# Kernel optimization log

Measured on AMD Instinct MI355X. Metric: run time of the kernel, lower is better.

## Reference

```python
import jax, jax.numpy as jnp
import numpy as np
from jax import lax

# module hyperparams (from init_kwargs)
K = 7
STRIDE = 1
PAD = 3
DIL = 1


def setup_inputs() -> dict:
    key = jax.random.key(0)
    ks = jax.random.split(key, 5)
    B, Cin, Cout, L = 4, 256, 256, 8192
    x = jax.random.normal(ks[0], (B, Cin, L), jnp.float32)
    # main conv weight (Cout, Cin, K), kaiming-ish scale
    weight = jax.random.normal(ks[1], (Cout, Cin, K), jnp.float32) * (1.0 / np.sqrt(Cin * K))
    bias = jax.random.normal(ks[2], (Cout,), jnp.float32) * 0.01
    # offset conv: Conv1d(Cin -> K, kernel K); small values so sampling is perturbed but in-range
    offset_w = jax.random.normal(ks[3], (K, Cin, K), jnp.float32) * 0.01
    offset_b = jax.random.normal(ks[4], (K,), jnp.float32) * 0.01
    return {"x": x, "weight": weight, "bias": bias, "offset_w": offset_w, "offset_b": offset_b}


def reference(x, weight, bias, offset_w, offset_b):
    B, Cin, L = x.shape
    out_len = (L + 2 * PAD - DIL * (K - 1) - 1) // STRIDE + 1

    # offset conv: (B, Cin, L) -> (B, K, out_len)
    offsets = lax.conv_general_dilated(
        x, offset_w, window_strides=(STRIDE,), padding=[(PAD, PAD)],
        rhs_dilation=(DIL,), dimension_numbers=("NCH", "OIH", "NCH"))
    offsets = offsets + offset_b[None, :, None]
    offsets = jnp.transpose(offsets, (0, 2, 1))  # (B, out_len, K)

    # standard sampling locations (1, out_len, K), shifted by padding as in original
    p = jnp.arange(out_len, dtype=jnp.float32)[None, :, None] * STRIDE
    p_k = (jnp.arange(K, dtype=jnp.float32) - (K - 1) / 2.0) * DIL
    loc = p + p_k[None, None, :] + PAD + offsets  # (B, out_len, K)

    # linear interpolation (clamped endpoints, matching torch clamp order)
    x0 = jnp.floor(loc).astype(jnp.int32)
    x1 = x0 + 1
    x0c = jnp.clip(x0, 0, L - 1)
    x1c = jnp.clip(x1, 0, L - 1)
    wa = x1c.astype(jnp.float32) - loc  # weights use clamped indices, as original
    wb = loc - x0c.astype(jnp.float32)

    # gather: per batch, (Cin, L)[:, (out_len, K)] -> (Cin, out_len, K)
    gather = jax.vmap(lambda xb, ib: xb[:, ib])
    fa = gather(x, x0c)  # (B, Cin, out_len, K)
    fb = gather(x, x1c)
    interp = wa[:, None] * fa + wb[:, None] * fb  # (B, Cin, out_len, K)

    # einsum 'blki,oik->blo' with interp laid out as (B, i=Cin, l, k)
    out = jnp.einsum("bilk,oik->bol", interp, weight) + bias[None, :, None]
    return out
```

## Files before the change

kernel.cpp:

```cpp
#include <hip/hip_runtime.h>
#include <hip/hip_bf16.h>


#define B_    4
#define CIN   256
#define COUT  256
#define LEN   8192
#define KK    7
#define NTOT  (B_ * LEN)
#define QTOT  (CIN * KK)
#define LPITCH 232

typedef short s16x8 __attribute__((ext_vector_type(8)));
typedef int   s32x4 __attribute__((ext_vector_type(4)));
typedef float f32x4 __attribute__((ext_vector_type(4)));

static __device__ __forceinline__ unsigned f2bf(float f) {
  union { float f; unsigned u; } u; u.f = f;
  unsigned r = u.u + 0x7FFF + ((u.u >> 16) & 1);
  return r >> 16;
}

static __device__ __forceinline__ int cvt_pk_bf16(float a, float b) {
  int r;
  asm("v_cvt_pk_bf16_f32 %0, %1, %2" : "=v"(r) : "v"(a), "v"(b));
  return r;
}

__global__ __launch_bounds__(256) void loc_partial(
    const float* __restrict__ X, const float* __restrict__ OW,
    float* __restrict__ Partial) {
  __shared__ float red[4][256][KK];

  const int t    = threadIdx.x;
  const int lane = t & 63;
  const int wu   = __builtin_amdgcn_readfirstlane(t >> 6);
  const int cg   = blockIdx.x >> 7;
  const int nb   = (blockIdx.x & 127) << 8;
  const int b    = nb >> 13;
  const int l0   = nb & (LEN - 1);

  float acc[KK][4];
#pragma unroll
  for (int k = 0; k < KK; ++k)
#pragma unroll
    for (int r = 0; r < 4; ++r) acc[k][r] = 0.0f;

#pragma unroll 2
  for (int ii = 0; ii < 16; ++ii) {
    const int i = cg * 64 + wu * 16 + ii;
    float owv[49];
#pragma unroll
    for (int k = 0; k < KK; ++k)
#pragma unroll
      for (int j = 0; j < KK; ++j)
        owv[k * 7 + j] = OW[(k * CIN + i) * KK + j];

    const float* xr = X + ((size_t)(b * CIN + i) << 13);
#pragma unroll
    for (int r = 0; r < 4; ++r) {
      const int lr = l0 + lane + 64 * r;
      float xv[KK];
#pragma unroll
      for (int j = 0; j < KK; ++j) {
        int pos = lr + j - 3;
        xv[j] = ((unsigned)pos < LEN) ? xr[pos] : 0.0f;
      }
#pragma unroll
      for (int k = 0; k < KK; ++k)
#pragma unroll
        for (int j = 0; j < KK; ++j)
          acc[k][r] += xv[j] * owv[k * 7 + j];
    }
  }

#pragma unroll
  for (int k = 0; k < KK; ++k)
#pragma unroll
    for (int r = 0; r < 4; ++r) red[wu][lane + 64 * r][k] = acc[k][r];
  __syncthreads();

#pragma unroll
  for (int k = 0; k < KK; ++k) {
    float s = red[0][t][k] + red[1][t][k] + red[2][t][k] + red[3][t][k];
    Partial[((size_t)(cg * 7 + k) << 15) + nb + t] = s;
  }
}

__global__ __launch_bounds__(256) void loc_reduce(
    const float* __restrict__ Partial, const float* __restrict__ OB,
    float* __restrict__ Loc) {
  int n = blockIdx.x * 256 + threadIdx.x;
  int l = n & (LEN - 1);
#pragma unroll
  for (int k = 0; k < KK; ++k) {
    float s = (float)(l + k) + OB[k];
#pragma unroll
    for (int cg = 0; cg < 4; ++cg)
      s += Partial[((size_t)(cg * 7 + k) << 15) + n];
    Loc[((size_t)k << 15) + n] = s;
  }
}

__global__ __launch_bounds__(256) void wt_build(
    const float* __restrict__ W, unsigned short* __restrict__ Wf) {
  __shared__ float Wl[16 * 32 * KK];
  const int t  = threadIdx.x;
  const int ot = blockIdx.x >> 3;
  const int c  = blockIdx.x & 7;

  for (int e = t; e < 16 * 32 * KK; e += 256) {
    int o = e / 224;
    int r = e - o * 224;
    Wl[e] = W[(size_t)(ot * 16 + o) * QTOT + c * 224 + r];
  }
  __syncthreads();

  const int lane = t & 63;
  const int sg   = t >> 6;
  const int ol   = lane & 15;
  const int ig   = lane >> 4;
  for (int s = sg; s < KK; s += 4) {
    s16x8 v;
#pragma unroll
    for (int j = 0; j < 8; ++j)
      v[j] = (short)f2bf(Wl[ol * 224 + (ig * 8 + j) * KK + s]);
    int f = (ot * 8 + c) * KK + s;
    *(s16x8*)(Wf + ((size_t)f << 9) + (lane << 3)) = v;
  }
}

__global__ __launch_bounds__(512, 2) void main_kernel(
    const float* __restrict__ X, const unsigned short* __restrict__ Wf,
    const float* __restrict__ Bias, const float* __restrict__ Loc,
    float* __restrict__ Out) {
  __shared__ unsigned short Il[2][64][LPITCH];

  const int t    = threadIdx.x;
  const int lane = t & 63;
  const int w    = t >> 6;
  const int n0   = blockIdx.x << 6;
  const int b    = n0 >> 13;
  const float* Xb = X + ((size_t)b << 21);

  const bool stager = (t < 448);
  const int nl = t & 63;
  const int kt = t >> 6;

  float c0 = 0.f, c1 = 0.f;
  const float* xp = Xb;
  if (stager) {
    float locv = Loc[((size_t)kt << 15) + n0 + nl];
    int x0  = (int)floorf(locv);
    int x0c = min(max(x0, 0), LEN - 1);
    int x1c = min(max(x0 + 1, 0), LEN - 1);
    float wa = (float)x1c - locv;
    float wb = locv - (float)x0c;
    bool hi = (x0 >= LEN - 1);
    bool lo = (x0 < 0);
    c0 = (hi ? 0.f : wa) + (lo ? wb : 0.f);
    c1 = (hi ? wa : 0.f) + (lo ? 0.f : wb);
    xp = Xb + min(max(x0, 0), LEN - 2);
  }

  f32x4 acc[2][4];
#pragma unroll
  for (int a = 0; a < 2; ++a)
#pragma unroll
    for (int cc = 0; cc < 4; ++cc) acc[a][cc] = (f32x4){0.f, 0.f, 0.f, 0.f};

  const int mrow = lane & 15;
  const int quad = lane >> 4;

  float f0[8], f1[8];

#define GATHER_Q(chunk, q)                                        \
  if (stager) {                                                   \
    _Pragma("unroll")                                             \
    for (int m = 0; m < 8; ++m) {                                 \
      const float* xr = xp + ((size_t)((chunk) * 32 + (q) * 8 + m) << 13); \
      f0[m] = xr[0];                                              \
      f1[m] = xr[1];                                              \
    }                                                             \
  }

#define CVT_Q(dst, q)                                             \
  if (stager) {                                                   \
    s32x4 vv;                                                     \
    _Pragma("unroll")                                             \
    for (int m = 0; m < 4; ++m) {                                 \
      float a = c0 * f0[2 * m]     + c1 * f1[2 * m];              \
      float d = c0 * f0[2 * m + 1] + c1 * f1[2 * m + 1];          \
      vv[m] = cvt_pk_bf16(a, d);                                  \
    }                                                             \
    *(s32x4*)((dst) + nl * LPITCH + kt * 32 + (q) * 8) = vv;      \
  }

#define AFL(ttv, sv)                                              \
  (*(const s16x8*)(Wf + ((size_t)(((w * 2 + (ttv)) * 8 + c) * KK + (sv)) << 9) + (lane << 3)))

#define MSTEP(sv, a0, a1) {                                                        \
    const s16x8 b0 = *(const s16x8*)(Icur + (mrow)      * LPITCH + (sv) * 32 + quad * 8); \
    const s16x8 b1 = *(const s16x8*)(Icur + (16 + mrow) * LPITCH + (sv) * 32 + quad * 8); \
    acc[0][0] = __builtin_amdgcn_mfma_f32_16x16x32_bf16(a0, b0, acc[0][0], 0, 0, 0); \
    acc[1][0] = __builtin_amdgcn_mfma_f32_16x16x32_bf16(a1, b0, acc[1][0], 0, 0, 0); \
    acc[0][1] = __builtin_amdgcn_mfma_f32_16x16x32_bf16(a0, b1, acc[0][1], 0, 0, 0); \
    acc[1][1] = __builtin_amdgcn_mfma_f32_16x16x32_bf16(a1, b1, acc[1][1], 0, 0, 0); \
    const s16x8 b2 = *(const s16x8*)(Icur + (32 + mrow) * LPITCH + (sv) * 32 + quad * 8); \
    const s16x8 b3 = *(const s16x8*)(Icur + (48 + mrow) * LPITCH + (sv) * 32 + quad * 8); \
    acc[0][2] = __builtin_amdgcn_mfma_f32_16x16x32_bf16(a0, b2, acc[0][2], 0, 0, 0); \
    acc[1][2] = __builtin_amdgcn_mfma_f32_16x16x32_bf16(a1, b2, acc[1][2], 0, 0, 0); \
    acc[0][3] = __builtin_amdgcn_mfma_f32_16x16x32_bf16(a0, b3, acc[0][3], 0, 0, 0); \
    acc[1][3] = __builtin_amdgcn_mfma_f32_16x16x32_bf16(a1, b3, acc[1][3], 0, 0, 0); \
  }

  {
    unsigned short* I0 = &Il[0][0][0];
    GATHER_Q(0, 0) CVT_Q(I0, 0)
    GATHER_Q(0, 1) CVT_Q(I0, 1)
    GATHER_Q(0, 2) CVT_Q(I0, 2)
    GATHER_Q(0, 3) CVT_Q(I0, 3)
  }
  __syncthreads();

  for (int c = 0; c < 8; ++c) {
    const int cur = c & 1;
    const unsigned short* Icur = &Il[cur][0][0];
    unsigned short*       Inxt = &Il[cur ^ 1][0][0];

    s16x8 afA[2][4];
#pragma unroll
    for (int tt = 0; tt < 2; ++tt)
#pragma unroll
      for (int s = 0; s < 4; ++s) afA[tt][s] = AFL(tt, s);
    __builtin_amdgcn_sched_barrier(0);

    if (c < 7) { GATHER_Q(c + 1, 0) }
    MSTEP(0, afA[0][0], afA[1][0])
    if (c < 7) { CVT_Q(Inxt, 0) GATHER_Q(c + 1, 1) }
    MSTEP(1, afA[0][1], afA[1][1])

    s16x8 afB[2][3];
#pragma unroll
    for (int tt = 0; tt < 2; ++tt)
#pragma unroll
      for (int s = 0; s < 3; ++s) afB[tt][s] = AFL(tt, 4 + s);
    __builtin_amdgcn_sched_barrier(0);

    if (c < 7) { CVT_Q(Inxt, 1) GATHER_Q(c + 1, 2) }
    MSTEP(2, afA[0][2], afA[1][2])
    if (c < 7) { CVT_Q(Inxt, 2) GATHER_Q(c + 1, 3) }
    MSTEP(3, afA[0][3], afA[1][3])
    if (c < 7) { CVT_Q(Inxt, 3) }
    MSTEP(4, afB[0][0], afB[1][0])
    MSTEP(5, afB[0][1], afB[1][1])
    MSTEP(6, afB[0][2], afB[1][2])
    if (c < 7) __syncthreads();
  }
#undef GATHER_Q
#undef CVT_Q
#undef AFL
#undef MSTEP

  const int lbase = (n0 & (LEN - 1)) + mrow;
#pragma unroll
  for (int tt = 0; tt < 2; ++tt) {
    const int obase = (w * 2 + tt) * 16 + quad * 4;
#pragma unroll
    for (int r = 0; r < 4; ++r) {
      const int o = obase + r;
      const float bv = Bias[o];
      float* orow = Out + (((size_t)(b * COUT + o)) << 13) + lbase;
#pragma unroll
      for (int nt = 0; nt < 4; ++nt)
        orow[nt * 16] = acc[tt][nt][r] + bv;
    }
  }
}

extern "C" void kernel_launch(void* const* d_in, const int* in_sizes, int n_in,
                              void* d_out, int out_size, void* d_ws, size_t ws_size,
                              hipStream_t stream) {
  const float* X    = (const float*)d_in[0];
  const float* W    = (const float*)d_in[1];
  const float* Bias = (const float*)d_in[2];
  const float* OW   = (const float*)d_in[3];
  const float* OB   = (const float*)d_in[4];
  float* Out = (float*)d_out;

  float* Loc = (float*)d_ws;
  unsigned short* Wf = (unsigned short*)(Loc + (size_t)NTOT * KK);
  float* Partial = (float*)(Wf + (size_t)COUT * QTOT);

  loc_partial<<<4 * 128, 256, 0, stream>>>(X, OW, Partial);
  loc_reduce<<<NTOT / 256, 256, 0, stream>>>(Partial, OB, Loc);
  wt_build<<<128, 256, 0, stream>>>(W, Wf);
  main_kernel<<<NTOT / 64, 512, 0, stream>>>(X, Wf, Bias, Loc, Out);
}
```

Before: 172.8 us.

## Gather interpolation taps with 8-byte-aligned vector loads and swizzle LDS staging

Each stager thread now loads a 4-float window aligned to an even address with one vector load per channel, in place of two scalar loads. The window offset is folded into four per-thread coefficients d0..d3, so the interpolation becomes a 4-term dot product. LDS writes and MFMA operand reads also use an XOR swizzle on the 8-element column group, meant to reduce bank conflicts. This cuts load instruction count at the cost of more FMAs and twice the fetched bytes per tap, and the swizzle must stay consistent between writer and reader.

```diff
diff --git a/kernel.cpp b/kernel.cpp
--- a/kernel.cpp
+++ b/kernel.cpp
@@ -14,6 +14,7 @@
 typedef short s16x8 __attribute__((ext_vector_type(8)));
 typedef int   s32x4 __attribute__((ext_vector_type(4)));
 typedef float f32x4 __attribute__((ext_vector_type(4)));
+typedef f32x4 f32x4a8 __attribute__((aligned(8)));
 
 static __device__ __forceinline__ unsigned f2bf(float f) {
   union { float f; unsigned u; } u; u.f = f;
@@ -147,8 +148,8 @@
   const int nl = t & 63;
   const int kt = t >> 6;
 
-  float c0 = 0.f, c1 = 0.f;
-  const float* xp = Xb;
+  int p0 = 0;
+  float d0 = 0.f, d1 = 0.f, d2 = 0.f, d3 = 0.f;
   if (stager) {
     float locv = Loc[((size_t)kt << 15) + n0 + nl];
     int x0  = (int)floorf(locv);
@@ -158,9 +159,15 @@
     float wb = locv - (float)x0c;
     bool hi = (x0 >= LEN - 1);
     bool lo = (x0 < 0);
-    c0 = (hi ? 0.f : wa) + (lo ? wb : 0.f);
-    c1 = (hi ? wa : 0.f) + (lo ? 0.f : wb);
-    xp = Xb + min(max(x0, 0), LEN - 2);
+    float c0 = (hi ? 0.f : wa) + (lo ? wb : 0.f);
+    float c1 = (hi ? wa : 0.f) + (lo ? 0.f : wb);
+    int xc = min(max(x0, 0), LEN - 2);
+    p0 = min(xc & ~1, LEN - 4);
+    int off = xc - p0;
+    d0 = (off == 0) ? c0 : 0.f;
+    d1 = (off == 1) ? c0 : ((off == 0) ? c1 : 0.f);
+    d2 = (off == 2) ? c0 : ((off == 1) ? c1 : 0.f);
+    d3 = (off == 2) ? c1 : 0.f;
   }
 
   f32x4 acc[2][4];
@@ -172,16 +179,19 @@
   const int mrow = lane & 15;
   const int quad = lane >> 4;
 
-  float f0[8], f1[8];
+  const int mr3  = mrow >> 3;
+  const int snl3 = ((nl >> 3) & 3) << 3;
+  const int qxA  = (quad << 3) ^ ((mr3 & 3) << 3);
+  const int qxB  = (quad << 3) ^ (((2 + mr3) & 3) << 3);
+
+  f32x4 fv[8];
 
 #define GATHER_Q(chunk, q)                                        \
   if (stager) {                                                   \
     _Pragma("unroll")                                             \
-    for (int m = 0; m < 8; ++m) {                                 \
-      const float* xr = xp + ((size_t)((chunk) * 32 + (q) * 8 + m) << 13); \
-      f0[m] = xr[0];                                              \
-      f1[m] = xr[1];                                              \
-    }                                                             \
+    for (int m = 0; m < 8; ++m)                                   \
+      fv[m] = *(const f32x4a8*)(Xb + p0 +                         \
+               (((chunk) * 32 + (q) * 8 + m) << 13));             \
   }
 
 #define CVT_Q(dst, q)                                             \
@@ -189,25 +199,26 @@
     s32x4 vv;                                                     \
     _Pragma("unroll")                                             \
     for (int m = 0; m < 4; ++m) {                                 \
-      float a = c0 * f0[2 * m]     + c1 * f1[2 * m];              \
-      float d = c0 * f0[2 * m + 1] + c1 * f1[2 * m + 1];          \
-      vv[m] = cvt_pk_bf16(a, d);                                  \
+      f32x4 u = fv[2 * m], v = fv[2 * m + 1];                     \
+      float a = d0 * u[0] + d1 * u[1] + d2 * u[2] + d3 * u[3];    \
+      float e = d0 * v[0] + d1 * v[1] + d2 * v[2] + d3 * v[3];    \
+      vv[m] = cvt_pk_bf16(a, e);                                  \
     }                                                             \
-    *(s32x4*)((dst) + nl * LPITCH + kt * 32 + (q) * 8) = vv;      \
+    *(s32x4*)((dst) + nl * LPITCH + kt * 32 + (((q) << 3) ^ snl3)) = vv; \
   }
 
 #define AFL(ttv, sv)                                              \
   (*(const s16x8*)(Wf + ((size_t)(((w * 2 + (ttv)) * 8 + c) * KK + (sv)) << 9) + (lane << 3)))
 
 #define MSTEP(sv, a0, a1) {                                                        \
-    const s16x8 b0 = *(const s16x8*)(Icur + (mrow)      * LPITCH + (sv) * 32 + quad * 8); \
-    const s16x8 b1 = *(const s16x8*)(Icur + (16 + mrow) * LPITCH + (sv) * 32 + quad * 8); \
+    const s16x8 b0 = *(const s16x8*)(Icur + (mrow)      * LPITCH + (sv) * 32 + qxA); \
+    const s16x8 b1 = *(const s16x8*)(Icur + (16 + mrow) * LPITCH + (sv) * 32 + qxB); \
     acc[0][0] = __builtin_amdgcn_mfma_f32_16x16x32_bf16(a0, b0, acc[0][0], 0, 0, 0); \
     acc[1][0] = __builtin_amdgcn_mfma_f32_16x16x32_bf16(a1, b0, acc[1][0], 0, 0, 0); \
     acc[0][1] = __builtin_amdgcn_mfma_f32_16x16x32_bf16(a0, b1, acc[0][1], 0, 0, 0); \
     acc[1][1] = __builtin_amdgcn_mfma_f32_16x16x32_bf16(a1, b1, acc[1][1], 0, 0, 0); \
-    const s16x8 b2 = *(const s16x8*)(Icur + (32 + mrow) * LPITCH + (sv) * 32 + quad * 8); \
-    const s16x8 b3 = *(const s16x8*)(Icur + (48 + mrow) * LPITCH + (sv) * 32 + quad * 8); \
+    const s16x8 b2 = *(const s16x8*)(Icur + (32 + mrow) * LPITCH + (sv) * 32 + qxA); \
+    const s16x8 b3 = *(const s16x8*)(Icur + (48 + mrow) * LPITCH + (sv) * 32 + qxB); \
     acc[0][2] = __builtin_amdgcn_mfma_f32_16x16x32_bf16(a0, b2, acc[0][2], 0, 0, 0); \
     acc[1][2] = __builtin_amdgcn_mfma_f32_16x16x32_bf16(a1, b2, acc[1][2], 0, 0, 0); \
     acc[0][3] = __builtin_amdgcn_mfma_f32_16x16x32_bf16(a0, b3, acc[0][3], 0, 0, 0); \
```

Measured after the change: 174.5 us. Within noise of the previous version (+1.0%).

## Fuse offset-conv partial and reduce kernels into one in-block reduction

Applied to the files above, without the earlier changes.

Replaces the two-kernel offset computation (channel-group partial sums written to a workspace, then a separate reduce kernel) with a single kernel. Each 512-thread block covers 64 positions, and its 8 waves split all 256 input channels before reducing through shared memory. This removes the Partial buffer round trip and one launch. In exchange it uses more blocks with fewer positions per thread, so the offset weights are reloaded per channel for each 64-position block instead of amortised over 256 positions.

```diff
diff --git a/kernel.cpp b/kernel.cpp
--- a/kernel.cpp
+++ b/kernel.cpp
@@ -27,78 +27,57 @@
   return r;
 }
 
-__global__ __launch_bounds__(256) void loc_partial(
+__global__ __launch_bounds__(512) void loc_fused(
     const float* __restrict__ X, const float* __restrict__ OW,
-    float* __restrict__ Partial) {
-  __shared__ float red[4][256][KK];
+    const float* __restrict__ OB, float* __restrict__ Loc) {
+  __shared__ float red[8][64][KK];
 
   const int t    = threadIdx.x;
   const int lane = t & 63;
-  const int wu   = __builtin_amdgcn_readfirstlane(t >> 6);
-  const int cg   = blockIdx.x >> 7;
-  const int nb   = (blockIdx.x & 127) << 8;
-  const int b    = nb >> 13;
-  const int l0   = nb & (LEN - 1);
-
-  float acc[KK][4];
-#pragma unroll
-  for (int k = 0; k < KK; ++k)
-#pragma unroll
-    for (int r = 0; r < 4; ++r) acc[k][r] = 0.0f;
+  const int g    = __builtin_amdgcn_readfirstlane(t >> 6);
+  const int n0   = blockIdx.x << 6;
+  const int b    = n0 >> 13;
+  const int l0   = n0 & (LEN - 1);
+  const float* Xb = X + ((size_t)b << 21);
+
+  float acc[KK];
+#pragma unroll
+  for (int k = 0; k < KK; ++k) acc[k] = 0.f;
 
 #pragma unroll 2
-  for (int ii = 0; ii < 16; ++ii) {
-    const int i = cg * 64 + wu * 16 + ii;
+  for (int ii = 0; ii < 32; ++ii) {
+    const int i = g * 32 + ii;
     float owv[49];
 #pragma unroll
     for (int k = 0; k < KK; ++k)
 #pragma unroll
       for (int j = 0; j < KK; ++j)
         owv[k * 7 + j] = OW[(k * CIN + i) * KK + j];
-
-    const float* xr = X + ((size_t)(b * CIN + i) << 13);
-#pragma unroll
-    for (int r = 0; r < 4; ++r) {
-      const int lr = l0 + lane + 64 * r;
-      float xv[KK];
-#pragma unroll
-      for (int j = 0; j < KK; ++j) {
-        int pos = lr + j - 3;
-        xv[j] = ((unsigned)pos < LEN) ? xr[pos] : 0.0f;
-      }
-#pragma unroll
-      for (int k = 0; k < KK; ++k)
-#pragma unroll
-        for (int j = 0; j < KK; ++j)
-          acc[k][r] += xv[j] * owv[k * 7 + j];
+    const float* xr = Xb + ((size_t)i << 13);
+    float xv[KK];
+#pragma unroll
+    for (int j = 0; j < KK; ++j) {
+      int pos = l0 + lane + j - 3;
+      xv[j] = ((unsigned)pos < LEN) ? xr[pos] : 0.0f;
     }
-  }
-
-#pragma unroll
-  for (int k = 0; k < KK; ++k)
-#pragma unroll
-    for (int r = 0; r < 4; ++r) red[wu][lane + 64 * r][k] = acc[k][r];
+#pragma unroll
+    for (int k = 0; k < KK; ++k)
+#pragma unroll
+      for (int j = 0; j < KK; ++j)
+        acc[k] += xv[j] * owv[k * 7 + j];
+  }
+
+#pragma unroll
+  for (int k = 0; k < KK; ++k) red[g][lane][k] = acc[k];
   __syncthreads();
 
-#pragma unroll
-  for (int k = 0; k < KK; ++k) {
-    float s = red[0][t][k] + red[1][t][k] + red[2][t][k] + red[3][t][k];
-    Partial[((size_t)(cg * 7 + k) << 15) + nb + t] = s;
-  }
-}
-
-__global__ __launch_bounds__(256) void loc_reduce(
-    const float* __restrict__ Partial, const float* __restrict__ OB,
-    float* __restrict__ Loc) {
-  int n = blockIdx.x * 256 + threadIdx.x;
-  int l = n & (LEN - 1);
-#pragma unroll
-  for (int k = 0; k < KK; ++k) {
-    float s = (float)(l + k) + OB[k];
-#pragma unroll
-    for (int cg = 0; cg < 4; ++cg)
-      s += Partial[((size_t)(cg * 7 + k) << 15) + n];
-    Loc[((size_t)k << 15) + n] = s;
+  if (t < 448) {
+    const int kt = t >> 6;
+    const int nl = t & 63;
+    float s = (float)(l0 + nl + kt) + OB[kt];
+#pragma unroll
+    for (int gg = 0; gg < 8; ++gg) s += red[gg][nl][kt];
+    Loc[((size_t)kt << 15) + n0 + nl] = s;
   }
 }
 
@@ -290,10 +269,8 @@
 
   float* Loc = (float*)d_ws;
   unsigned short* Wf = (unsigned short*)(Loc + (size_t)NTOT * KK);
-  float* Partial = (float*)(Wf + (size_t)COUT * QTOT);
-
-  loc_partial<<<4 * 128, 256, 0, stream>>>(X, OW, Partial);
-  loc_reduce<<<NTOT / 256, 256, 0, stream>>>(Partial, OB, Loc);
+
+  loc_fused<<<NTOT / 64, 512, 0, stream>>>(X, OW, OB, Loc);
   wt_build<<<128, 256, 0, stream>>>(W, Wf);
   main_kernel<<<NTOT / 64, 512, 0, stream>>>(X, Wf, Bias, Loc, Out);
 }
```

Measured after the change: 202.6 us. 17.3% more time.
